# Performance work log

Hardware: AMD Instinct MI355X
Metric: run time of the kernel (lower is better)

Reference implementation:

```python
import jax, jax.numpy as jnp
import numpy as np
from jax.scipy.linalg import expm

EPS = 1e-5  # torch LayerNorm default

def _layernorm(x, g, b):
    m = x.mean(-1, keepdims=True)
    v = ((x - m) ** 2).mean(-1, keepdims=True)
    return (x - m) / jnp.sqrt(v + EPS) * g + b

def setup_inputs() -> dict:
    H, S, K = 1024, 64, 3
    B, T = 4, 4096
    key = jax.random.key(0)
    ks = jax.random.split(key, 12)
    sc = 0.02
    inp = {
        'x': jax.random.normal(ks[0], (B, T, H), jnp.float32),
        'A': -jnp.abs(jax.random.normal(ks[1], (S, S), jnp.float32) * sc),
        'dt_A': jnp.asarray(0.1, jnp.float32),
        'B_w': jax.random.normal(ks[2], (S, H), jnp.float32) * sc,
        'B_b': jnp.zeros((S,), jnp.float32),
        'C_w': jax.random.normal(ks[3], (S, H), jnp.float32) * sc,
        'C_b': jnp.zeros((S,), jnp.float32),
        'D_w': jax.random.normal(ks[4], (H, S), jnp.float32) * sc,
        'D_b': jnp.zeros((H,), jnp.float32),
        'conv_w': jax.random.normal(ks[5], (H, 1, K), jnp.float32) * sc,  # depthwise
        'conv_b': jnp.zeros((H,), jnp.float32),
        'gate_w': jax.random.normal(ks[6], (2 * H, H), jnp.float32) * sc,
        'gate_b': jnp.zeros((2 * H,), jnp.float32),
        'ln_in_g': jnp.ones((H,), jnp.float32),
        'ln_in_b': jnp.zeros((H,), jnp.float32),
        'ln_st_g': jnp.ones((S,), jnp.float32),
        'ln_st_b': jnp.zeros((S,), jnp.float32),
    }
    return inp

def reference(x, A, dt_A, B_w, B_b, C_w, C_b, D_w, D_b, conv_w, conv_b,
              gate_w, gate_b, ln_in_g, ln_in_b, ln_st_g, ln_st_b):
    Bt, T, H = x.shape
    K = conv_w.shape[-1]
    pad = K // 2
    x_norm = _layernorm(x, ln_in_g, ln_in_b)  # [B,T,H]
    # depthwise conv1d (groups = H), 'same' padding, residual add
    xc = jnp.transpose(x_norm, (0, 2, 1))  # [B,H,T]
    xc = jax.lax.conv_general_dilated(
        xc, conv_w, window_strides=(1,), padding=[(pad, pad)],
        dimension_numbers=('NCH', 'OIH', 'NCH'), feature_group_count=H)
    xc = xc + conv_b[None, :, None]
    x_norm = x_norm + jnp.transpose(xc, (0, 2, 1))
    # gating
    gate_all = x_norm @ gate_w.T + gate_b  # [B,T,2H]
    gate, input_gate = gate_all[..., :H], gate_all[..., H:]
    gate = jax.nn.sigmoid(gate)
    # input-dependent B, C
    Bm = (x_norm * jax.nn.sigmoid(input_gate)) @ B_w.T + B_b  # [B,T,S]
    Cm = x_norm @ C_w.T + C_b                                  # [B,T,S]
    A_bar = expm(dt_A * A)  # [S,S]
    # sequential recurrence over time via scan
    def step(state, bc):
        b_t, c_t = bc
        s = state @ A_bar + b_t
        s = _layernorm(s, ln_st_g, ln_st_b)
        return s, c_t * s
    state0 = jnp.zeros((Bt, A.shape[0]), x.dtype)
    _, ys = jax.lax.scan(step, state0,
                         (jnp.transpose(Bm, (1, 0, 2)), jnp.transpose(Cm, (1, 0, 2))))
    ssm = jnp.transpose(ys, (1, 0, 2))  # [B,T,S]
    ssm = ssm @ D_w.T + D_b             # [B,T,H]
    return ssm * gate
```

## Files before the change

### kernel.cpp

```cpp
#include <hip/hip_runtime.h>
#include <cstdint>

#define EPS 1e-5f
typedef float f32x4 __attribute__((ext_vector_type(4)));
typedef short bf8 __attribute__((ext_vector_type(8)));
typedef unsigned short u16;
typedef unsigned short u16x8 __attribute__((ext_vector_type(8)));
typedef unsigned int uint4v __attribute__((ext_vector_type(4)));

__device__ __forceinline__ u16 f2b(float f){
  unsigned x = __float_as_uint(f);
  unsigned r = x + 0x7FFFu + ((x>>16)&1u);
  return (u16)(r>>16);
}
__device__ __forceinline__ float b2f(u16 h){ return __uint_as_float(((unsigned)h)<<16); }
__device__ __forceinline__ unsigned pk2(float a, float b){
  unsigned ua = __float_as_uint(a) + 0x8000u;
  unsigned ub = __float_as_uint(b) + 0x8000u;
  return __builtin_amdgcn_perm(ub, ua, 0x07060302u);
}

#define GLL(gp, lp) __builtin_amdgcn_global_load_lds((__attribute__((address_space(1))) const void*)(gp), (__attribute__((address_space(3))) void*)(lp), 16, 0, 0)

__global__ __launch_bounds__(1024) void k_prep(const float* __restrict__ A, const float* __restrict__ dtp,
    const float* __restrict__ stg, const float* __restrict__ stb,
    float* __restrict__ abeta, u16* __restrict__ ft)
{
  __shared__ float M[4096], Ta[4096], Tb[4096], P[4096];
  __shared__ float cmn[64];
  int tid = threadIdx.x;
  float dt = dtp[0];
  for (int e=tid; e<4096; e+=1024){
    float v = dt * A[e];
    int i = e>>6, j = e&63;
    M[e] = v;
    P[e] = v + (i==j ? 1.0f : 0.0f);
    Ta[e] = v;
  }
  __syncthreads();
  float* src = Ta; float* dst = Tb;
  for (int k=2;k<=14;k++){
    float inv = 1.0f/(float)k;
    int i = tid>>4, j0 = (tid&15)*4;
    float a0=0,a1=0,a2=0,a3=0;
    for (int m2=0;m2<64;m2++){
      float f = src[i*64+m2];
      const float* Mr = &M[m2*64+j0];
      a0 += f*Mr[0]; a1 += f*Mr[1]; a2 += f*Mr[2]; a3 += f*Mr[3];
    }
    a0*=inv; a1*=inv; a2*=inv; a3*=inv;
    int base=i*64+j0;
    dst[base+0]=a0; dst[base+1]=a1; dst[base+2]=a2; dst[base+3]=a3;
    P[base+0]+=a0; P[base+1]+=a1; P[base+2]+=a2; P[base+3]+=a3;
    __syncthreads();
    float* tmp=src; src=dst; dst=tmp;
  }
  if (tid<64){
    float c0=0, ab=0; int p = tid;
    for (int q2=0;q2<64;q2++){ float ap = P[q2*64+p]; c0 += stg[q2]*ap; ab += stb[q2]*ap; }
    cmn[p] = c0*(1.0f/64.0f);
    abeta[p] = ab;
  }
  __syncthreads();
  for (int e=tid; e<4096; e+=1024){
    int q2=e>>6, p=e&63;
    Ta[e] = stg[q2]*P[q2*64+p] - cmn[p];
  }
  __syncthreads();
  for (int ii=0; ii<4; ii++){
    int e = tid*4+ii;
    int j = e&7, l = (e>>3)&63, kt=(e>>9)&1, mt=e>>10;
    int q2 = 16*(2*kt + (j>>2)) + 4*(l>>4) + (j&3);
    int p = 16*mt + (l&15);
    float v = Ta[q2*64+p];
    u16 hi = f2b(v);
    float lo = v - b2f(hi);
    ft[e] = hi;
    ft[e+4096] = f2b(lo);
  }
}

__global__ __launch_bounds__(256) void k_wcvt(const float* __restrict__ gw, const float* __restrict__ bw,
   const float* __restrict__ cw, const float* __restrict__ dw,
   u16* __restrict__ ogw, u16* __restrict__ obw, u16* __restrict__ ocw, u16* __restrict__ odw)
{
  int n = blockIdx.x*256 + threadIdx.x;
  if (n < 2097152) ogw[n] = f2b(gw[n]);
  else if (n < 2162688) obw[n-2097152] = f2b(bw[n-2097152]);
  else if (n < 2228224) ocw[n-2162688] = f2b(cw[n-2162688]);
  else odw[n-2228224] = f2b(dw[n-2228224]);
}

__global__ __launch_bounds__(256) void k_lnconv(const float* __restrict__ x, const float* __restrict__ gin,
  const float* __restrict__ bin, const float* __restrict__ cwt, const float* __restrict__ cb, u16* __restrict__ xn)
{
  __shared__ float red[10][8];
  int tid = threadIdx.x; int w = tid>>6; int lane = tid&63;
  int r0 = blockIdx.x*8;
  int bt = r0>>12, t0 = r0&4095;
  int c4 = tid*4;
  f32x4 g4 = *(const f32x4*)(gin + c4);
  f32x4 b4 = *(const f32x4*)(bin + c4);
  f32x4 vals[10];
  for (int lr=0; lr<10; lr++){
    int t = t0 - 1 + lr;
    f32x4 xv = {0,0,0,0};
    bool ok = (t>=0 && t<4096);
    if (ok) xv = *(const f32x4*)(x + (size_t)(bt*4096+t)*1024 + c4);
    float s = xv.x+xv.y+xv.z+xv.w;
    float q = xv.x*xv.x+xv.y*xv.y+xv.z*xv.z+xv.w*xv.w;
    for (int m2=1;m2<=32;m2<<=1){ s += __shfl_xor(s,m2,64); q += __shfl_xor(q,m2,64); }
    if (lane==0){ red[lr][w]=s; red[lr][4+w]=q; }
    __syncthreads();
    s = red[lr][0]+red[lr][1]+red[lr][2]+red[lr][3];
    q = red[lr][4]+red[lr][5]+red[lr][6]+red[lr][7];
    float mu = s*(1.f/1024.f);
    float var = q*(1.f/1024.f) - mu*mu;
    float rr = rsqrtf(var + EPS);
    f32x4 o = {0,0,0,0};
    if (ok){
      o.x=(xv.x-mu)*rr*g4.x+b4.x; o.y=(xv.y-mu)*rr*g4.y+b4.y;
      o.z=(xv.z-mu)*rr*g4.z+b4.z; o.w=(xv.w-mu)*rr*g4.w+b4.w;
    }
    vals[lr]=o;
  }
  float w0[4], w1[4], w2[4], cbv[4];
  for (int ii=0;ii<4;ii++){ int c = c4+ii; w0[ii]=cwt[c*3+0]; w1[ii]=cwt[c*3+1]; w2[ii]=cwt[c*3+2]; cbv[ii]=cb[c]; }
  for (int lr=1; lr<=8; lr++){
    int t = t0 + lr - 1;
    f32x4 o;
    o.x = vals[lr].x + w0[0]*vals[lr-1].x + w1[0]*vals[lr].x + w2[0]*vals[lr+1].x + cbv[0];
    o.y = vals[lr].y + w0[1]*vals[lr-1].y + w1[1]*vals[lr].y + w2[1]*vals[lr+1].y + cbv[1];
    o.z = vals[lr].z + w0[2]*vals[lr-1].z + w1[2]*vals[lr].z + w2[2]*vals[lr+1].z + cbv[2];
    o.w = vals[lr].w + w0[3]*vals[lr-1].w + w1[3]*vals[lr].w + w2[3]*vals[lr+1].w + cbv[3];
    size_t off = (size_t)(bt*4096+t)*1024 + c4;
    unsigned lo2 = (unsigned)f2b(o.x) | ((unsigned)f2b(o.y)<<16);
    unsigned hi2 = (unsigned)f2b(o.z) | ((unsigned)f2b(o.w)<<16);
    uint2 pk; pk.x=lo2; pk.y=hi2;
    *(uint2*)(xn + off) = pk;
  }
}

__global__ __launch_bounds__(256) void k_gate(const u16* __restrict__ xn, const u16* __restrict__ gw,
    const float* __restrict__ gb, u16* __restrict__ gate_o, u16* __restrict__ xg_o)
{
  __shared__ char smem[33792];
  u16* As = (u16*)smem;
  u16* Bs = (u16*)(smem + 8192);
  float* st = (float*)smem;
  int tid=threadIdx.x, w=tid>>6, l=tid&63;
  int flat = blockIdx.x + (int)gridDim.x*blockIdx.y;
  int logical = (flat&7)*256 + (flat>>3);
  int n0 = (logical&15)*128, m0 = (logical>>4)*128;
  int wr = w>>1, wc = w&1;
  f32x4 acc[4][4] = {};
  for (int kk=0; kk<32; kk++){
    int k0 = kk*32;
    for (int i2=0;i2<2;i2++){
      const char* ga = (const char*)xn + ((size_t)(m0+32*w+16*i2+(l>>2))*1024 + k0)*2 + (l&3)*16;
      GLL(ga, (char*)As + (32*w+16*i2)*64);
      const char* gbp = (const char*)gw + ((size_t)(n0+32*w+16*i2+(l>>2))*1024 + k0)*2 + (l&3)*16;
      GLL(gbp, (char*)Bs + (32*w+16*i2)*64);
    }
    __syncthreads();
    bf8 af[4], bfr[4];
    for (int mt=0;mt<4;mt++) af[mt] = *(const bf8*)(As + (wr*64+mt*16+(l&15))*32 + 8*(l>>4));
    for (int nt=0;nt<4;nt++) bfr[nt] = *(const bf8*)(Bs + (wc*64+nt*16+(l&15))*32 + 8*(l>>4));
    for (int mt=0;mt<4;mt++) for (int nt=0;nt<4;nt++)
      acc[mt][nt] = __builtin_amdgcn_mfma_f32_16x16x32_bf16(af[mt], bfr[nt], acc[mt][nt], 0,0,0);
    __syncthreads();
  }
  bool isxg = (n0 >= 1024);
  int r2 = tid>>2, q = tid&3;
  f32x4 gb4[8];
  for (int j=0;j<8;j++) gb4[j] = *(const f32x4*)(gb + n0 + q*32 + j*4);
  int g = l>>4, c = l&15;
  for (int p=0;p<2;p++){
    __syncthreads();
    if (wr==p){
      for (int mt=0;mt<4;mt++) for (int nt=0;nt<4;nt++)
        for (int r=0;r<4;r++)
          st[(mt*16+4*g+r)*132 + wc*64+nt*16+c] = acc[mt][nt][r];
    }
    __syncthreads();
    int row = m0 + p*64 + r2;
    const float* sp = st + r2*132 + q*32;
    u16 ob[32];
    if (!isxg){
      for (int j=0;j<8;j++){
        f32x4 v = *(const f32x4*)(sp + 4*j);
        v = v + gb4[j];
        ob[4*j+0] = f2b(1.0f/(1.0f+__expf(-v.x)));
        ob[4*j+1] = f2b(1.0f/(1.0f+__expf(-v.y)));
        ob[4*j+2] = f2b(1.0f/(1.0f+__expf(-v.z)));
        ob[4*j+3] = f2b(1.0f/(1.0f+__expf(-v.w)));
      }
    } else {
      const u16* xp = xn + (size_t)row*1024 + (n0-1024) + q*32;
      u16 xb[32];
      for (int j=0;j<4;j++){
        u16x8 t8 = *(const u16x8*)(xp + 8*j);
        for (int e=0;e<8;e++) xb[8*j+e] = t8[e];
      }
      for (int j=0;j<8;j++){
        f32x4 v = *(const f32x4*)(sp + 4*j);
        v = v + gb4[j];
        ob[4*j+0] = f2b(b2f(xb[4*j+0]) * (1.0f/(1.0f+__expf(-v.x))));
        ob[4*j+1] = f2b(b2f(xb[4*j+1]) * (1.0f/(1.0f+__expf(-v.y))));
        ob[4*j+2] = f2b(b2f(xb[4*j+2]) * (1.0f/(1.0f+__expf(-v.z))));
        ob[4*j+3] = f2b(b2f(xb[4*j+3]) * (1.0f/(1.0f+__expf(-v.w))));
      }
    }
    u16* op = isxg ? (xg_o + (size_t)row*1024 + (n0-1024) + q*32)
                   : (gate_o + (size_t)row*1024 + n0 + q*32);
    unsigned od[16];
    for (int i2=0;i2<16;i2++) od[i2] = (unsigned)ob[2*i2] | ((unsigned)ob[2*i2+1]<<16);
    uint4v s0 = {od[0],od[1],od[2],od[3]};
    uint4v s1 = {od[4],od[5],od[6],od[7]};
    uint4v s2 = {od[8],od[9],od[10],od[11]};
    uint4v s3 = {od[12],od[13],od[14],od[15]};
    *(uint4v*)(op+ 0) = s0;
    *(uint4v*)(op+ 8) = s1;
    *(uint4v*)(op+16) = s2;
    *(uint4v*)(op+24) = s3;
  }
}

__global__ __launch_bounds__(256) void k_bc(const u16* __restrict__ xg, const u16* __restrict__ xn,
   const u16* __restrict__ bw, const u16* __restrict__ cw,
   const float* __restrict__ bb, const float* __restrict__ cbias_, const float* __restrict__ abeta,
   float* __restrict__ c_ws, u16* __restrict__ cm)
{
  __shared__ u16 As[128*32], Bs[64*32];
  int tid=threadIdx.x, w=tid>>6, l=tid&63;
  int id = blockIdx.x; int half = id>>7; int m0 = (id&127)*128;
  const u16* Ap = half ? xn : xg;
  const u16* Bp = half ? cw : bw;
  f32x4 acc[2][4]={};
  for (int kk=0;kk<32;kk++){
    int k0=kk*32;
    for (int i2=0;i2<2;i2++){
      const char* ga=(const char*)Ap + ((size_t)(m0+32*w+16*i2+(l>>2))*1024+k0)*2+(l&3)*16;
      GLL(ga, (char*)As+(32*w+16*i2)*64);
    }
    { const char* gbp=(const char*)Bp + ((size_t)(16*w+(l>>2))*1024+k0)*2+(l&3)*16;
      GLL(gbp, (char*)Bs+(16*w)*64); }
    __syncthreads();
    bf8 af[2], bfr[4];
    for (int mt=0;mt<2;mt++) af[mt]=*(const bf8*)(As+(32*w+16*mt+(l&15))*32+8*(l>>4));
    for (int nt=0;nt<4;nt++) bfr[nt]=*(const bf8*)(Bs+(16*nt+(l&15))*32+8*(l>>4));
    for (int mt=0;mt<2;mt++) for(int nt=0;nt<4;nt++)
      acc[mt][nt]=__builtin_amdgcn_mfma_f32_16x16x32_bf16(af[mt],bfr[nt],acc[mt][nt],0,0,0);
    __syncthreads();
  }
  int g=l>>4, c=l&15;
  if (half==0){
    for (int nt=0;nt<4;nt++){ int n=16*nt+c; float bias=bb[n]; float ab=abeta[n];
      for(int mt=0;mt<2;mt++) for(int r=0;r<4;r++){
        int row=m0+32*w+16*mt+4*g+r; int bt=row>>12, t=row&4095;
        float v=acc[mt][nt][r]+bias + (t>0?ab:0.0f);
        c_ws[(size_t)t*256 + bt*64 + n] = v;
      }
    }
  } else {
    for (int nt=0;nt<4;nt++){ int n=16*nt+c; float bias=cbias_[n];
      for(int mt=0;mt<2;mt++) for(int r=0;r<4;r++){
        int row=m0+32*w+16*mt+4*g+r;
        cm[(size_t)row*64+n]=f2b(acc[mt][nt][r]+bias);
      }
    }
  }
}

__global__ __launch_bounds__(64,1) void k_scan(const float* __restrict__ c_ws, const u16* __restrict__ ft,
  float* __restrict__ z_ws)
{
  __shared__ float ring[16*256];
  int l=threadIdx.x, g=l>>4, b=l&3;
  const bf8* ftv=(const bf8*)ft;
  bf8 Wh[4][2], Wl[4][2];
  for(int mt=0;mt<4;mt++)for(int kt=0;kt<2;kt++){
    Wh[mt][kt]=ftv[(mt*2+kt)*64+l];
    Wl[mt][kt]=ftv[(8+mt*2+kt)*64+l];
  }
  const f32x4 zed = {0.f,0.f,0.f,0.f};
  f32x4 z0,z1,z2,z3;
  {
    const float* zp = c_ws + b*64 + 4*g;
    z0=*(const f32x4*)(zp+0); z1=*(const f32x4*)(zp+16); z2=*(const f32x4*)(zp+32); z3=*(const f32x4*)(zp+48);
  }
  for(int u2=1;u2<=8;u2++){
    const char* ga=(const char*)c_ws + (size_t)u2*1024 + l*16;
    GLL(ga, (char*)ring + u2*1024);
  }
  asm volatile("s_waitcnt vmcnt(0)" ::: "memory");
  unsigned laneoff;
  {
    __attribute__((address_space(3))) float* l3=( __attribute__((address_space(3))) float*)ring;
    laneoff=(unsigned)(uintptr_t)l3 + (unsigned)(b*256 + g*16);
  }
  unsigned voff = (unsigned)(((l&15)*64 + 4*g)*4);
  unsigned long long zb = (unsigned long long)(uintptr_t)z_ws;
  f32x4 cN0,cN1,cN2,cN3;
  bf8 zf0, zf1;

  {
    uint4v p0,p1;
    p0.x=pk2(z0.x,z0.y); p0.y=pk2(z0.z,z0.w); p0.z=pk2(z1.x,z1.y); p0.w=pk2(z1.z,z1.w);
    p1.x=pk2(z2.x,z2.y); p1.y=pk2(z2.z,z2.w); p1.z=pk2(z3.x,z3.y); p1.w=pk2(z3.z,z3.w);
    { union { uint4v u; bf8 h; } cv; cv.u=p0; zf0=cv.h; cv.u=p1; zf1=cv.h; }
  }

  unsigned slotr = 1024u;
  unsigned ldst  = 9u*1024u;
  const char* gsrc = (const char*)c_ws + (size_t)9*1024;

  for (int t=0; t<4096; ++t){
    asm volatile("s_waitcnt vmcnt(24)" ::: "memory");
    { unsigned ro = laneoff + slotr;
      asm volatile("ds_read_b128 %0, %4 offset:0\n\t"
                   "ds_read_b128 %1, %4 offset:64\n\t"
                   "ds_read_b128 %2, %4 offset:128\n\t"
                   "ds_read_b128 %3, %4 offset:192"
                   : "=v"(cN0),"=v"(cN1),"=v"(cN2),"=v"(cN3) : "v"(ro) : "memory"); }
    GLL(gsrc + (size_t)l*16, (char*)ring + ldst);
    f32x4 u0=__builtin_amdgcn_mfma_f32_16x16x32_bf16(Wh[0][0],zf0,zed,0,0,0);
    f32x4 u1=__builtin_amdgcn_mfma_f32_16x16x32_bf16(Wh[1][0],zf0,zed,0,0,0);
    f32x4 u2=__builtin_amdgcn_mfma_f32_16x16x32_bf16(Wh[2][0],zf0,zed,0,0,0);
    f32x4 u3=__builtin_amdgcn_mfma_f32_16x16x32_bf16(Wh[3][0],zf0,zed,0,0,0);
    u0=__builtin_amdgcn_mfma_f32_16x16x32_bf16(Wh[0][1],zf1,u0,0,0,0);
    u1=__builtin_amdgcn_mfma_f32_16x16x32_bf16(Wh[1][1],zf1,u1,0,0,0);
    u2=__builtin_amdgcn_mfma_f32_16x16x32_bf16(Wh[2][1],zf1,u2,0,0,0);
    u3=__builtin_amdgcn_mfma_f32_16x16x32_bf16(Wh[3][1],zf1,u3,0,0,0);
    u0=__builtin_amdgcn_mfma_f32_16x16x32_bf16(Wl[0][0],zf0,u0,0,0,0);
    u1=__builtin_amdgcn_mfma_f32_16x16x32_bf16(Wl[1][0],zf0,u1,0,0,0);
    u2=__builtin_amdgcn_mfma_f32_16x16x32_bf16(Wl[2][0],zf0,u2,0,0,0);
    u3=__builtin_amdgcn_mfma_f32_16x16x32_bf16(Wl[3][0],zf0,u3,0,0,0);
    u0=__builtin_amdgcn_mfma_f32_16x16x32_bf16(Wl[0][1],zf1,u0,0,0,0);
    u1=__builtin_amdgcn_mfma_f32_16x16x32_bf16(Wl[1][1],zf1,u1,0,0,0);
    u2=__builtin_amdgcn_mfma_f32_16x16x32_bf16(Wl[2][1],zf1,u2,0,0,0);
    u3=__builtin_amdgcn_mfma_f32_16x16x32_bf16(Wl[3][1],zf1,u3,0,0,0);
    float rr;
    {
      f32x4 s4=(z0+z1)+(z2+z3);
      float s=(s4.x+s4.y)+(s4.z+s4.w);
      f32x4 qa=z0*z0; qa=z1*z1+qa;
      f32x4 qb=z2*z2; qb=z3*z3+qb;
      f32x4 q4=qa+qb;
      float q=(q4.x+q4.y)+(q4.z+q4.w);
      float sB=s, qB=q;
      asm("v_permlane16_swap_b32 %0, %1" : "+v"(s), "+v"(sB));
      asm("v_permlane16_swap_b32 %0, %1" : "+v"(q), "+v"(qB));
      s+=sB; q+=qB;
      float sC=s, qC=q;
      asm("v_permlane32_swap_b32 %0, %1" : "+v"(s), "+v"(sC));
      asm("v_permlane32_swap_b32 %0, %1" : "+v"(q), "+v"(qC));
      s+=sC; q+=qC;
      float mu=s*(1.f/64.f);
      float var=q*(1.f/64.f)-mu*mu;
      rr=rsqrtf(var+EPS);
    }
    asm volatile("global_store_dwordx4 %0, %1, %5\n\t"
                 "global_store_dwordx4 %0, %2, %5 offset:64\n\t"
                 "global_store_dwordx4 %0, %3, %5 offset:128\n\t"
                 "global_store_dwordx4 %0, %4, %5 offset:192"
                 :: "v"(voff), "v"(z0), "v"(z1), "v"(z2), "v"(z3), "s"(zb) : "memory");
    voff += 4096u;
    slotr = (slotr + 1024u) & 16383u;
    ldst  = (ldst  + 1024u) & 16383u;
    gsrc += 1024;
    asm volatile("s_waitcnt lgkmcnt(0)" : "+v"(cN0),"+v"(cN1),"+v"(cN2),"+v"(cN3) :: "memory");
    z0 = u0*rr + cN0;
    z1 = u1*rr + cN1;
    z2 = u2*rr + cN2;
    z3 = u3*rr + cN3;
    uint4v p0,p1;
    p0.x=pk2(z0.x,z0.y); p0.y=pk2(z0.z,z0.w); p0.z=pk2(z1.x,z1.y); p0.w=pk2(z1.z,z1.w);
    p1.x=pk2(z2.x,z2.y); p1.y=pk2(z2.z,z2.w); p1.z=pk2(z3.x,z3.y); p1.w=pk2(z3.z,z3.w);
    { union { uint4v u; bf8 h; } cv; cv.u=p0; zf0=cv.h; cv.u=p1; zf1=cv.h; }
  }
}

__global__ __launch_bounds__(256) void k_y(const float* __restrict__ z_ws, const u16* __restrict__ cm,
  const float* __restrict__ stg, const float* __restrict__ stb, u16* __restrict__ y)
{
  int tid=threadIdx.x, w=tid>>6, l=tid&63;
  int token = blockIdx.x*4 + w;
  int bt = token>>12, t = token&4095;
  float zv = z_ws[(size_t)t*1024 + bt*64 + l];
  float s=zv, q=zv*zv;
  for (int m2=1;m2<=32;m2<<=1){ s += __shfl_xor(s,m2,64); q += __shfl_xor(q,m2,64); }
  float mu=s*(1.f/64.f), var=q*(1.f/64.f)-mu*mu, rr=rsqrtf(var+EPS);
  float sv=(zv-mu)*rr*stg[l]+stb[l];
  y[(size_t)token*64 + l] = f2b(sv * b2f(cm[(size_t)token*64+l]));
}

__global__ __launch_bounds__(256) void k_out(const u16* __restrict__ y, const u16* __restrict__ dw,
   const float* __restrict__ db, const u16* __restrict__ gate, float* __restrict__ out)
{
  __shared__ float tr[4][16][68];
  int tid=threadIdx.x, w=tid>>6, l=tid&63, g=l>>4, c=l&15;
  int n0=blockIdx.x*64, m0=blockIdx.y*64;
  int mrow = m0 + 16*w + c;
  bf8 af0=*(const bf8*)(y + (size_t)mrow*64 + 8*g);
  bf8 af1=*(const bf8*)(y + (size_t)mrow*64 + 32 + 8*g);
  f32x4 acc[4];
  for(int nt=0;nt<4;nt++){
    int n=n0+16*nt+c;
    bf8 b0=*(const bf8*)(dw + (size_t)n*64 + 8*g);
    bf8 b1=*(const bf8*)(dw + (size_t)n*64 + 32 + 8*g);
    f32x4 a={0,0,0,0};
    a=__builtin_amdgcn_mfma_f32_16x16x32_bf16(af0,b0,a,0,0,0);
    a=__builtin_amdgcn_mfma_f32_16x16x32_bf16(af1,b1,a,0,0,0);
    acc[nt]=a+db[n];
  }
  for(int nt=0;nt<4;nt++) for(int r=0;r<4;r++) tr[w][4*g+r][16*nt+c]=acc[nt][r];
  __syncthreads();
  int lr=l>>2, cc0=(l&3)*16;
  int grow=m0+16*w+lr;
  const u16* gp = gate + (size_t)grow*1024 + n0 + cc0;
  u16x8 g0=*(const u16x8*)(gp), g1=*(const u16x8*)(gp+8);
  float* op = out + (size_t)grow*1024 + n0 + cc0;
  float vv[16];
  for(int j2=0;j2<16;j2++){
    u16 gb16 = (j2<8)? g0[j2] : g1[j2-8];
    vv[j2]=tr[w][lr][cc0+j2]*b2f(gb16);
  }
  for(int j2=0;j2<4;j2++){
    f32x4 ov={vv[4*j2],vv[4*j2+1],vv[4*j2+2],vv[4*j2+3]};
    *(f32x4*)(op+4*j2)=ov;
  }
}

extern "C" void kernel_launch(void* const* d_in, const int* in_sizes, int n_in,
                              void* d_out, int out_size, void* d_ws, size_t ws_size,
                              hipStream_t stream) {
  const float* x=(const float*)d_in[0];
  const float* A=(const float*)d_in[1];
  const float* dt=(const float*)d_in[2];
  const float* B_w=(const float*)d_in[3];
  const float* B_b=(const float*)d_in[4];
  const float* C_w=(const float*)d_in[5];
  const float* C_b=(const float*)d_in[6];
  const float* D_w=(const float*)d_in[7];
  const float* D_b=(const float*)d_in[8];
  const float* conv_w=(const float*)d_in[9];
  const float* conv_b=(const float*)d_in[10];
  const float* gate_w=(const float*)d_in[11];
  const float* gate_b=(const float*)d_in[12];
  const float* ln_in_g=(const float*)d_in[13];
  const float* ln_in_b=(const float*)d_in[14];
  const float* ln_st_g=(const float*)d_in[15];
  const float* ln_st_b=(const float*)d_in[16];
  char* ws=(char*)d_ws;
  u16* xn   =(u16*)(ws);
  u16* xg   =(u16*)(ws+33554432);
  u16* gate =(u16*)(ws+67108864);
  u16* gwb  =(u16*)(ws+100663296);
  u16* bwb  =(u16*)(ws+104857600);
  u16* cwb  =(u16*)(ws+104988672);
  u16* dwb  =(u16*)(ws+105119744);
  u16* cm   =(u16*)(ws+105250816);
  float* c_ws=(float*)(ws+107347968);
  float* z_ws=(float*)(ws+111558656);
  u16* y    =(u16*)(ws+128335872);
  float* abeta=(float*)(ws+130433024);
  u16* ft   =(u16*)(ws+130433280);
  float* out=(float*)d_out;

  hipLaunchKernelGGL(k_prep,  dim3(1),      dim3(1024),0,stream, A, dt, ln_st_g, ln_st_b, abeta, ft);
  hipLaunchKernelGGL(k_wcvt,  dim3(8960),   dim3(256), 0,stream, gate_w,B_w,C_w,D_w, gwb,bwb,cwb,dwb);
  hipLaunchKernelGGL(k_lnconv,dim3(2048),   dim3(256), 0,stream, x, ln_in_g, ln_in_b, conv_w, conv_b, xn);
  hipLaunchKernelGGL(k_gate,  dim3(16,128), dim3(256), 0,stream, xn,gwb,gate_b,gate,xg);
  hipLaunchKernelGGL(k_bc,    dim3(256),    dim3(256), 0,stream, xg,xn,bwb,cwb,B_b,C_b,abeta,c_ws,cm);
  hipLaunchKernelGGL(k_scan,  dim3(1),      dim3(64),  0,stream, c_ws, ft, z_ws);
  hipLaunchKernelGGL(k_y,     dim3(4096),   dim3(256), 0,stream, z_ws,cm,ln_st_g,ln_st_b,y);
  hipLaunchKernelGGL(k_out,   dim3(16,256), dim3(256), 0,stream, y,dwb,D_b,gate,out);
}
```

Measured before the change: 1.718 ms.

## Split scan matrix into bf16 off-diagonal part plus fp32 diagonal and mean terms

The recurrence matrix used in the sequential scan is decomposed. The diagonal and the LayerNorm mean-correction rank-1 term are applied exactly in fp32 vector ops, and only the off-diagonal remainder goes through a single bf16 MFMA pass. This halves the MFMAs on the serial critical path per timestep (8 instead of 16 hi/lo split MFMAs). The trade-off is lower precision on the off-diagonal entries and a few extra FMAs per step.

```diff
diff --git a/kernel.cpp b/kernel.cpp
--- a/kernel.cpp
+++ b/kernel.cpp
@@ -24,7 +24,7 @@
 
 __global__ __launch_bounds__(1024) void k_prep(const float* __restrict__ A, const float* __restrict__ dtp,
     const float* __restrict__ stg, const float* __restrict__ stb,
-    float* __restrict__ abeta, u16* __restrict__ ft)
+    float* __restrict__ abeta, u16* __restrict__ ft, float* __restrict__ dcm)
 {
   __shared__ float M[4096], Ta[4096], Tb[4096], P[4096];
   __shared__ float cmn[64];
@@ -60,11 +60,13 @@
     for (int q2=0;q2<64;q2++){ float ap = P[q2*64+p]; c0 += stg[q2]*ap; ab += stb[q2]*ap; }
     cmn[p] = c0*(1.0f/64.0f);
     abeta[p] = ab;
+    dcm[p]    = stg[p]*P[p*64+p];
+    dcm[64+p] = c0*(1.0f/64.0f);
   }
   __syncthreads();
   for (int e=tid; e<4096; e+=1024){
     int q2=e>>6, p=e&63;
-    Ta[e] = stg[q2]*P[q2*64+p] - cmn[p];
+    Ta[e] = stg[q2]*P[q2*64+p];
   }
   __syncthreads();
   for (int ii=0; ii<4; ii++){
@@ -72,11 +74,8 @@
     int j = e&7, l = (e>>3)&63, kt=(e>>9)&1, mt=e>>10;
     int q2 = 16*(2*kt + (j>>2)) + 4*(l>>4) + (j&3);
     int p = 16*mt + (l&15);
-    float v = Ta[q2*64+p];
-    u16 hi = f2b(v);
-    float lo = v - b2f(hi);
-    ft[e] = hi;
-    ft[e+4096] = f2b(lo);
+    float v = (q2==p) ? 0.0f : Ta[q2*64+p];
+    ft[e] = f2b(v);
   }
 }
 
@@ -273,15 +272,18 @@
 }
 
 __global__ __launch_bounds__(64,1) void k_scan(const float* __restrict__ c_ws, const u16* __restrict__ ft,
-  float* __restrict__ z_ws)
+  const float* __restrict__ dcm, float* __restrict__ z_ws)
 {
   __shared__ float ring[16*256];
   int l=threadIdx.x, g=l>>4, b=l&3;
   const bf8* ftv=(const bf8*)ft;
-  bf8 Wh[4][2], Wl[4][2];
-  for(int mt=0;mt<4;mt++)for(int kt=0;kt<2;kt++){
-    Wh[mt][kt]=ftv[(mt*2+kt)*64+l];
-    Wl[mt][kt]=ftv[(8+mt*2+kt)*64+l];
+  bf8 Rb[4][2];
+  for(int mt=0;mt<4;mt++)for(int kt=0;kt<2;kt++)
+    Rb[mt][kt]=ftv[(mt*2+kt)*64+l];
+  f32x4 D2r[4], Cm4[4];
+  for(int mt=0;mt<4;mt++){
+    D2r[mt] = *(const f32x4*)(dcm + 16*mt + 4*g);
+    Cm4[mt] = *(const f32x4*)(dcm + 64 + 16*mt + 4*g);
   }
   const f32x4 zed = {0.f,0.f,0.f,0.f};
   f32x4 z0,z1,z2,z3;
@@ -324,26 +326,18 @@
                    "ds_read_b128 %3, %4 offset:192"
                    : "=v"(cN0),"=v"(cN1),"=v"(cN2),"=v"(cN3) : "v"(ro) : "memory"); }
     GLL(gsrc + (size_t)l*16, (char*)ring + ldst);
-    f32x4 u0=__builtin_amdgcn_mfma_f32_16x16x32_bf16(Wh[0][0],zf0,zed,0,0,0);
-    f32x4 u1=__builtin_amdgcn_mfma_f32_16x16x32_bf16(Wh[1][0],zf0,zed,0,0,0);
-    f32x4 u2=__builtin_amdgcn_mfma_f32_16x16x32_bf16(Wh[2][0],zf0,zed,0,0,0);
-    f32x4 u3=__builtin_amdgcn_mfma_f32_16x16x32_bf16(Wh[3][0],zf0,zed,0,0,0);
-    u0=__builtin_amdgcn_mfma_f32_16x16x32_bf16(Wh[0][1],zf1,u0,0,0,0);
-    u1=__builtin_amdgcn_mfma_f32_16x16x32_bf16(Wh[1][1],zf1,u1,0,0,0);
-    u2=__builtin_amdgcn_mfma_f32_16x16x32_bf16(Wh[2][1],zf1,u2,0,0,0);
-    u3=__builtin_amdgcn_mfma_f32_16x16x32_bf16(Wh[3][1],zf1,u3,0,0,0);
-    u0=__builtin_amdgcn_mfma_f32_16x16x32_bf16(Wl[0][0],zf0,u0,0,0,0);
-    u1=__builtin_amdgcn_mfma_f32_16x16x32_bf16(Wl[1][0],zf0,u1,0,0,0);
-    u2=__builtin_amdgcn_mfma_f32_16x16x32_bf16(Wl[2][0],zf0,u2,0,0,0);
-    u3=__builtin_amdgcn_mfma_f32_16x16x32_bf16(Wl[3][0],zf0,u3,0,0,0);
-    u0=__builtin_amdgcn_mfma_f32_16x16x32_bf16(Wl[0][1],zf1,u0,0,0,0);
-    u1=__builtin_amdgcn_mfma_f32_16x16x32_bf16(Wl[1][1],zf1,u1,0,0,0);
-    u2=__builtin_amdgcn_mfma_f32_16x16x32_bf16(Wl[2][1],zf1,u2,0,0,0);
-    u3=__builtin_amdgcn_mfma_f32_16x16x32_bf16(Wl[3][1],zf1,u3,0,0,0);
-    float rr;
+    f32x4 u0=__builtin_amdgcn_mfma_f32_16x16x32_bf16(Rb[0][0],zf0,zed,0,0,0);
+    f32x4 u1=__builtin_amdgcn_mfma_f32_16x16x32_bf16(Rb[1][0],zf0,zed,0,0,0);
+    f32x4 u2=__builtin_amdgcn_mfma_f32_16x16x32_bf16(Rb[2][0],zf0,zed,0,0,0);
+    f32x4 u3=__builtin_amdgcn_mfma_f32_16x16x32_bf16(Rb[3][0],zf0,zed,0,0,0);
+    u0=__builtin_amdgcn_mfma_f32_16x16x32_bf16(Rb[0][1],zf1,u0,0,0,0);
+    u1=__builtin_amdgcn_mfma_f32_16x16x32_bf16(Rb[1][1],zf1,u1,0,0,0);
+    u2=__builtin_amdgcn_mfma_f32_16x16x32_bf16(Rb[2][1],zf1,u2,0,0,0);
+    u3=__builtin_amdgcn_mfma_f32_16x16x32_bf16(Rb[3][1],zf1,u3,0,0,0);
+    float s, rr;
     {
       f32x4 s4=(z0+z1)+(z2+z3);
-      float s=(s4.x+s4.y)+(s4.z+s4.w);
+      s=(s4.x+s4.y)+(s4.z+s4.w);
       f32x4 qa=z0*z0; qa=z1*z1+qa;
       f32x4 qb=z2*z2; qb=z3*z3+qb;
       f32x4 q4=qa+qb;
@@ -360,6 +354,11 @@
       float var=q*(1.f/64.f)-mu*mu;
       rr=rsqrtf(var+EPS);
     }
+    asm volatile("s_waitcnt lgkmcnt(0)" : "+v"(cN0),"+v"(cN1),"+v"(cN2),"+v"(cN3) :: "memory");
+    f32x4 h0 = (z0*D2r[0] - Cm4[0]*s)*rr + cN0;
+    f32x4 h1 = (z1*D2r[1] - Cm4[1]*s)*rr + cN1;
+    f32x4 h2 = (z2*D2r[2] - Cm4[2]*s)*rr + cN2;
+    f32x4 h3 = (z3*D2r[3] - Cm4[3]*s)*rr + cN3;
     asm volatile("global_store_dwordx4 %0, %1, %5\n\t"
                  "global_store_dwordx4 %0, %2, %5 offset:64\n\t"
                  "global_store_dwordx4 %0, %3, %5 offset:128\n\t"
@@ -369,11 +368,10 @@
     slotr = (slotr + 1024u) & 16383u;
     ldst  = (ldst  + 1024u) & 16383u;
     gsrc += 1024;
-    asm volatile("s_waitcnt lgkmcnt(0)" : "+v"(cN0),"+v"(cN1),"+v"(cN2),"+v"(cN3) :: "memory");
-    z0 = u0*rr + cN0;
-    z1 = u1*rr + cN1;
-    z2 = u2*rr + cN2;
-    z3 = u3*rr + cN3;
+    z0 = u0*rr + h0;
+    z1 = u1*rr + h1;
+    z2 = u2*rr + h2;
+    z3 = u3*rr + h3;
     uint4v p0,p1;
     p0.x=pk2(z0.x,z0.y); p0.y=pk2(z0.z,z0.w); p0.z=pk2(z1.x,z1.y); p0.w=pk2(z1.z,z1.w);
     p1.x=pk2(z2.x,z2.y); p1.y=pk2(z2.z,z2.w); p1.z=pk2(z3.x,z3.y); p1.w=pk2(z3.z,z3.w);
@@ -466,14 +464,15 @@
   u16* y    =(u16*)(ws+128335872);
   float* abeta=(float*)(ws+130433024);
   u16* ft   =(u16*)(ws+130433280);
+  float* dcm =(float*)(ws+130433280+8192);
   float* out=(float*)d_out;
 
-  hipLaunchKernelGGL(k_prep,  dim3(1),      dim3(1024),0,stream, A, dt, ln_st_g, ln_st_b, abeta, ft);
+  hipLaunchKernelGGL(k_prep,  dim3(1),      dim3(1024),0,stream, A, dt, ln_st_g, ln_st_b, abeta, ft, dcm);
   hipLaunchKernelGGL(k_wcvt,  dim3(8960),   dim3(256), 0,stream, gate_w,B_w,C_w,D_w, gwb,bwb,cwb,dwb);
   hipLaunchKernelGGL(k_lnconv,dim3(2048),   dim3(256), 0,stream, x, ln_in_g, ln_in_b, conv_w, conv_b, xn);
   hipLaunchKernelGGL(k_gate,  dim3(16,128), dim3(256), 0,stream, xn,gwb,gate_b,gate,xg);
   hipLaunchKernelGGL(k_bc,    dim3(256),    dim3(256), 0,stream, xg,xn,bwb,cwb,B_b,C_b,abeta,c_ws,cm);
-  hipLaunchKernelGGL(k_scan,  dim3(1),      dim3(64),  0,stream, c_ws, ft, z_ws);
+  hipLaunchKernelGGL(k_scan,  dim3(1),      dim3(64),  0,stream, c_ws, ft, dcm, z_ws);
   hipLaunchKernelGGL(k_y,     dim3(4096),   dim3(256), 0,stream, z_ws,cm,ln_st_g,ln_st_b,y);
   hipLaunchKernelGGL(k_out,   dim3(16,256), dim3(256), 0,stream, y,dwb,D_b,gate,out);
 }
```

Result: slower. 1.846 ms (+7.4%).
